# Performance work log

Hardware: AMD Instinct MI355X
Metric: run time of the kernel (lower is better)

The kernel has to match this reference:

```python
import jax, jax.numpy as jnp
import numpy as np

B, C, H, W = 4, 256, 48, 48
HEADS, DIM_HEAD, SCALE = 8, 64, 10.0
INNER = HEADS * DIM_HEAD
EPS = 1e-12


def setup_inputs() -> dict:
    key = jax.random.key(0)
    k1, k2, k3, k4 = jax.random.split(key, 4)
    x = jax.random.normal(k1, (B, C, H, W), dtype=jnp.float32)
    # 1x1 conv weights stored as [out_ch, in_ch]
    w_qkv = jax.random.normal(k2, (3 * INNER, C), dtype=jnp.float32) * (1.0 / np.sqrt(C))
    w_out = jax.random.normal(k3, (C, INNER), dtype=jnp.float32) * (1.0 / np.sqrt(INNER))
    b_out = jax.random.normal(k4, (C,), dtype=jnp.float32) * 0.01
    return {"x": x, "w_qkv": w_qkv, "w_out": w_out, "b_out": b_out}


def _l2norm(t):
    # normalize along last axis, clamping the norm at EPS (matches torch l2norm)
    denom = jnp.maximum(jnp.linalg.norm(t, axis=-1, keepdims=True), EPS)
    return t / denom


def reference(x, w_qkv, w_out, b_out):
    b, c, h, w = x.shape
    n = h * w
    # 1x1 conv QKV projection: [B, 3*INNER, H, W]
    qkv = jnp.einsum('oc,bchw->bohw', w_qkv, x)
    q, k, v = jnp.split(qkv, 3, axis=1)
    # [B, heads, dim_head, N] -> [B, heads, N, dim_head]
    def to_bhnd(t):
        return t.reshape(b, HEADS, DIM_HEAD, n).transpose(0, 1, 3, 2)
    q = _l2norm(to_bhnd(q))
    k = _l2norm(to_bhnd(k))
    v = to_bhnd(v)
    sim = jnp.einsum('bhid,bhjd->bhij', q, k) * SCALE  # [B,h,N,N]
    attn = jax.nn.softmax(sim, axis=-1)
    out = jnp.einsum('bhij,bhjd->bhid', attn, v)  # [B,h,N,d]
    # back to [B, INNER, H, W]
    out = out.transpose(0, 1, 3, 2).reshape(b, INNER, h, w)
    # 1x1 conv output projection with bias
    out = jnp.einsum('oc,bchw->bohw', w_out, out) + b_out[None, :, None, None]
    return out
```

## Files before the change

### kernel.cpp

```cpp
#include <hip/hip_runtime.h>

typedef unsigned short u16;
typedef __attribute__((ext_vector_type(8))) short bf16x8;
typedef __attribute__((ext_vector_type(4))) float f32x4;

#define MFMA16(A,B,C) __builtin_amdgcn_mfma_f32_16x16x32_bf16(A,B,C,0,0,0)

#define B_ 4
#define C_ 256
#define N_ 2304
#define HEADS_ 8
#define DH_ 64
#define INNER_ 512
#define SCALE_LOG2E 14.426950408889634f

__device__ __forceinline__ u16 f2bf(float f) {
    union { float f; unsigned int u; } v; v.f = f;
    unsigned int r = v.u + 0x7fffu + ((v.u >> 16) & 1u);
    return (u16)(r >> 16);
}
__device__ __forceinline__ unsigned int pk2(float a, float b) {
    union { float f; unsigned int u; } va, vb; va.f = a; vb.f = b;
    return __builtin_amdgcn_perm(vb.u + 0x8000u, va.u + 0x8000u, 0x07060302u);
}

__global__ __launch_bounds__(256) void k_prep(const float* __restrict__ x,
                                              u16* __restrict__ xT,
                                              const float* __restrict__ w_qkv,
                                              u16* __restrict__ wqb,
                                              const float* __restrict__ w_out,
                                              u16* __restrict__ wob) {
    __shared__ float tile[64][65];
    int idx = blockIdx.x;
    int t = threadIdx.x;
    if (idx < 576) {
        int b = idx / 144, rem = idx % 144;
        int n0 = (rem >> 2) * 64, c0 = (rem & 3) * 64;
        const float* xb = x + (size_t)b * C_ * N_;
        u16* xTb = xT + (size_t)b * N_ * C_;
        int r = t >> 4;
        int q4 = (t & 15) * 4;
#pragma unroll
        for (int pass = 0; pass < 4; ++pass) {
            int c = r + pass * 16;
            float4 v = *(const float4*)(xb + (size_t)(c0 + c) * N_ + n0 + q4);
            tile[c][q4+0] = v.x; tile[c][q4+1] = v.y; tile[c][q4+2] = v.z; tile[c][q4+3] = v.w;
        }
        __syncthreads();
#pragma unroll
        for (int pass = 0; pass < 4; ++pass) {
            int n = r + pass * 16;
            ushort4 o;
            o.x = f2bf(tile[q4+0][n]); o.y = f2bf(tile[q4+1][n]);
            o.z = f2bf(tile[q4+2][n]); o.w = f2bf(tile[q4+3][n]);
            *(ushort4*)(xTb + (size_t)(n0 + n) * C_ + c0 + q4) = o;
        }
    } else if (idx < 960) {
        int i = (idx - 576) * 256 + t;
        float4 v = ((const float4*)w_qkv)[i];
        ushort4 o;
        o.x = f2bf(v.x); o.y = f2bf(v.y); o.z = f2bf(v.z); o.w = f2bf(v.w);
        ((ushort4*)wqb)[i] = o;
    } else {
        int i = (idx - 960) * 256 + t;
        float4 v = ((const float4*)w_out)[i];
        ushort4 o;
        o.x = f2bf(v.x); o.y = f2bf(v.y); o.z = f2bf(v.z); o.w = f2bf(v.w);
        ((ushort4*)wob)[i] = o;
    }
}

__global__ __launch_bounds__(256) void k_qkv(const u16* __restrict__ w_qkv,
                                             const u16* __restrict__ xT,
                                             u16* __restrict__ Qn,
                                             u16* __restrict__ Kn,
                                             u16* __restrict__ Vt) {
    __shared__ __align__(16) u16 Wt[64][264];
    __shared__ __align__(16) u16 Xt[64][264];
    int mt = blockIdx.x, nt = blockIdx.y, b = blockIdx.z;
    int tid = threadIdx.x;
    int wv = tid >> 6, lane = tid & 63;
    int col = lane & 15, quad = lane >> 4;
    int o0 = mt * 64;
    const u16* wtile = w_qkv + (size_t)o0 * C_;
    const u16* xtile = xT + ((size_t)b * N_ + nt*64) * C_;
#pragma unroll
    for (int p = 0; p < 8; ++p) {
        int c = p * 256 + tid;
        int row = c >> 5, seg = c & 31;
        *(uint4*)(&Wt[row][seg*8]) = *(const uint4*)(wtile + (size_t)row * C_ + seg*8);
        *(uint4*)(&Xt[row][seg*8]) = *(const uint4*)(xtile + (size_t)row * C_ + seg*8);
    }
    __syncthreads();
    f32x4 z = {0.f, 0.f, 0.f, 0.f};
    f32x4 acc[4]; acc[0]=z; acc[1]=z; acc[2]=z; acc[3]=z;
#pragma unroll
    for (int ks = 0; ks < 8; ++ks) {
        bf16x8 bfrag = *(const bf16x8*)(&Xt[wv*16 + col][ks*32 + quad*8]);
#pragma unroll
        for (int mb = 0; mb < 4; ++mb) {
            bf16x8 afrag = *(const bf16x8*)(&Wt[mb*16 + col][ks*32 + quad*8]);
            acc[mb] = MFMA16(afrag, bfrag, acc[mb]);
        }
    }
    int n = nt * 64 + wv * 16 + col;
    int which = mt >> 3, h = mt & 7;
    if (which < 2) {
        float s = 0.f;
#pragma unroll
        for (int mb = 0; mb < 4; ++mb)
#pragma unroll
            for (int r = 0; r < 4; ++r) s += acc[mb][r] * acc[mb][r];
        s += __shfl_xor(s, 16);
        s += __shfl_xor(s, 32);
        float inv = 1.f / fmaxf(sqrtf(s), 1e-12f);
        u16* dst = (which == 0 ? Qn : Kn) + (((size_t)b * HEADS_ + h) * N_ + n) * DH_;
#pragma unroll
        for (int mb = 0; mb < 4; ++mb) {
            ushort4 o;
            o.x = f2bf(acc[mb][0] * inv); o.y = f2bf(acc[mb][1] * inv);
            o.z = f2bf(acc[mb][2] * inv); o.w = f2bf(acc[mb][3] * inv);
            *(ushort4*)(dst + mb*16 + quad*4) = o;
        }
    } else {
        u16* dst = Vt + ((size_t)b * HEADS_ + h) * (size_t)DH_ * N_;
#pragma unroll
        for (int mb = 0; mb < 4; ++mb)
#pragma unroll
            for (int r = 0; r < 4; ++r)
                dst[(size_t)(mb*16 + quad*4 + r) * N_ + n] = f2bf(acc[mb][r]);
    }
}

__global__ __launch_bounds__(256) void k_attn_split(const u16* __restrict__ Qn,
                                                    const u16* __restrict__ Kn,
                                                    const u16* __restrict__ Vt,
                                                    float* __restrict__ Op,
                                                    float* __restrict__ lp) {
    __shared__ __align__(16) u16 Kt[64][72];
    __shared__ __align__(16) u16 Vtl[64][72];
    __shared__ __align__(16) u16 plds[4][32][72];
    int head_lin = blockIdx.x & 31;
    int rest = blockIdx.x >> 5;
    int qt = rest % 18;
    int khalf = rest / 18;
    int b = head_lin >> 3, h = head_lin & 7;
    int tid = threadIdx.x;
    int wv = tid >> 6, lane = tid & 63;
    int col = lane & 15, quad = lane >> 4;
    size_t head = (size_t)b * HEADS_ + h;
    const u16* Qh = Qn + head * (size_t)N_ * DH_;
    const u16* Kh = Kn + head * (size_t)N_ * DH_ + (size_t)khalf * 1152 * DH_;
    const u16* Vh = Vt + head * (size_t)DH_ * N_;
    int q0 = qt * 128 + wv * 32;
    bf16x8 qfA0 = *(const bf16x8*)(Qh + (size_t)(q0 + col) * DH_ + quad*8);
    bf16x8 qfA1 = *(const bf16x8*)(Qh + (size_t)(q0 + col) * DH_ + 32 + quad*8);
    bf16x8 qfB0 = *(const bf16x8*)(Qh + (size_t)(q0 + 16 + col) * DH_ + quad*8);
    bf16x8 qfB1 = *(const bf16x8*)(Qh + (size_t)(q0 + 16 + col) * DH_ + 32 + quad*8);
    f32x4 z = {0.f, 0.f, 0.f, 0.f};
    f32x4 OA[4], OB[4];
#pragma unroll
    for (int i = 0; i < 4; ++i) { OA[i] = z; OB[i] = z; }
    float lA = 0.f, lB = 0.f;
    int srow = tid >> 3, sseg = tid & 7;
    const u16* ksrc0 = Kh + (size_t)tid * 8;
    const u16* vsrc0 = Vh + (size_t)srow * N_ + khalf * 1152 + sseg * 8;

    uint4 k0 = *(const uint4*)(ksrc0);
    uint4 k1 = *(const uint4*)(ksrc0 + 2048);
    uint4 v0 = *(const uint4*)(vsrc0);
    uint4 v1 = *(const uint4*)(vsrc0 + (size_t)32 * N_);

    for (int kt = 0; kt < 18; ++kt) {
        *(uint4*)(&Kt[srow][sseg*8])      = k0;
        *(uint4*)(&Kt[32 + srow][sseg*8]) = k1;
        *(uint4*)(&Vtl[srow][sseg*8])      = v0;
        *(uint4*)(&Vtl[32 + srow][sseg*8]) = v1;
        __syncthreads();
        int ktn = kt + 1 < 18 ? kt + 1 : kt;
        k0 = *(const uint4*)(ksrc0 + (size_t)ktn * 4096);
        k1 = *(const uint4*)(ksrc0 + (size_t)ktn * 4096 + 2048);
        v0 = *(const uint4*)(vsrc0 + ktn * 64);
        v1 = *(const uint4*)(vsrc0 + (size_t)32 * N_ + ktn * 64);
        float rsA = 0.f, rsB = 0.f;
#pragma unroll
        for (int nb = 0; nb < 4; ++nb) {
            bf16x8 kf0 = *(const bf16x8*)(&Kt[nb*16 + col][quad*8]);
            bf16x8 kf1 = *(const bf16x8*)(&Kt[nb*16 + col][32 + quad*8]);
            f32x4 a = MFMA16(kf0, qfA0, z);
            a = MFMA16(kf1, qfA1, a);
            f32x4 c = MFMA16(kf0, qfB0, z);
            c = MFMA16(kf1, qfB1, c);
            float a0 = exp2f(fmaf(a[0], SCALE_LOG2E, -SCALE_LOG2E));
            float a1 = exp2f(fmaf(a[1], SCALE_LOG2E, -SCALE_LOG2E));
            float a2 = exp2f(fmaf(a[2], SCALE_LOG2E, -SCALE_LOG2E));
            float a3 = exp2f(fmaf(a[3], SCALE_LOG2E, -SCALE_LOG2E));
            float c0 = exp2f(fmaf(c[0], SCALE_LOG2E, -SCALE_LOG2E));
            float c1 = exp2f(fmaf(c[1], SCALE_LOG2E, -SCALE_LOG2E));
            float c2 = exp2f(fmaf(c[2], SCALE_LOG2E, -SCALE_LOG2E));
            float c3 = exp2f(fmaf(c[3], SCALE_LOG2E, -SCALE_LOG2E));
            rsA += (a0 + a1) + (a2 + a3);
            rsB += (c0 + c1) + (c2 + c3);
            uint2 wA, wB;
            wA.x = pk2(a0, a1); wA.y = pk2(a2, a3);
            wB.x = pk2(c0, c1); wB.y = pk2(c2, c3);
            *(uint2*)(&plds[wv][col][nb*16 + quad*4]) = wA;
            *(uint2*)(&plds[wv][16 + col][nb*16 + quad*4]) = wB;
        }
        lA += rsA; lB += rsB;
        __asm__ volatile("" ::: "memory");
#pragma unroll
        for (int ks = 0; ks < 2; ++ks) {
            bf16x8 pfA = *(const bf16x8*)(&plds[wv][col][ks*32 + quad*8]);
            bf16x8 pfB = *(const bf16x8*)(&plds[wv][16 + col][ks*32 + quad*8]);
#pragma unroll
            for (int nb = 0; nb < 4; ++nb) {
                bf16x8 vf = *(const bf16x8*)(&Vtl[nb*16 + col][ks*32 + quad*8]);
                OA[nb] = MFMA16(vf, pfA, OA[nb]);
                OB[nb] = MFMA16(vf, pfB, OB[nb]);
            }
        }
        __asm__ volatile("" ::: "memory");
        __syncthreads();
    }
    lA += __shfl_xor(lA, 16); lA += __shfl_xor(lA, 32);
    lB += __shfl_xor(lB, 16); lB += __shfl_xor(lB, 32);
    float* dstA = Op + (((size_t)khalf * B_ + b) * N_ + q0 + col) * INNER_ + h * DH_;
    float* dstB = dstA + (size_t)16 * INNER_;
#pragma unroll
    for (int nb = 0; nb < 4; ++nb) {
        *(f32x4*)(dstA + nb*16 + quad*4) = OA[nb];
        *(f32x4*)(dstB + nb*16 + quad*4) = OB[nb];
    }
    if (quad == 0) {
        size_t lbase = (((size_t)khalf * B_ + b) * HEADS_ + h) * N_;
        lp[lbase + q0 + col] = lA;
        lp[lbase + q0 + 16 + col] = lB;
    }
}

__global__ __launch_bounds__(256) void k_comb(const float* __restrict__ Op,
                                              const float* __restrict__ lp,
                                              u16* __restrict__ AO) {
    int g = blockIdx.x * 256 + threadIdx.x;
    int b = g / 294912;
    int rem = g % 294912;
    int n = rem >> 7;
    int i4 = rem & 127;
    int h = i4 >> 4;
    float4 a = ((const float4*)Op)[g];
    float4 c = ((const float4*)Op)[g + 1179648];
    float l = lp[((size_t)b * HEADS_ + h) * N_ + n] +
              lp[(((size_t)B_ + b) * HEADS_ + h) * N_ + n];
    float inv = 1.f / l;
    ushort4 o;
    o.x = f2bf((a.x + c.x) * inv);
    o.y = f2bf((a.y + c.y) * inv);
    o.z = f2bf((a.z + c.z) * inv);
    o.w = f2bf((a.w + c.w) * inv);
    ((ushort4*)AO)[g] = o;
}

__global__ __launch_bounds__(256) void k_attn(const u16* __restrict__ Qn,
                                              const u16* __restrict__ Kn,
                                              const u16* __restrict__ Vt,
                                              u16* __restrict__ AO) {
    __shared__ __align__(16) u16 Kt[64][72];
    __shared__ __align__(16) u16 Vtl[64][72];
    __shared__ __align__(16) u16 plds[4][32][72];
    int head_lin = blockIdx.x & 31;
    int qt = blockIdx.x >> 5;
    int b = head_lin >> 3, h = head_lin & 7;
    int tid = threadIdx.x;
    int wv = tid >> 6, lane = tid & 63;
    int col = lane & 15, quad = lane >> 4;
    size_t head = (size_t)b * HEADS_ + h;
    const u16* Qh = Qn + head * (size_t)N_ * DH_;
    const u16* Kh = Kn + head * (size_t)N_ * DH_;
    const u16* Vh = Vt + head * (size_t)DH_ * N_;
    int q0 = qt * 128 + wv * 32;
    bf16x8 qfA0 = *(const bf16x8*)(Qh + (size_t)(q0 + col) * DH_ + quad*8);
    bf16x8 qfA1 = *(const bf16x8*)(Qh + (size_t)(q0 + col) * DH_ + 32 + quad*8);
    bf16x8 qfB0 = *(const bf16x8*)(Qh + (size_t)(q0 + 16 + col) * DH_ + quad*8);
    bf16x8 qfB1 = *(const bf16x8*)(Qh + (size_t)(q0 + 16 + col) * DH_ + 32 + quad*8);
    f32x4 z = {0.f, 0.f, 0.f, 0.f};
    f32x4 OA[4], OB[4];
#pragma unroll
    for (int i = 0; i < 4; ++i) { OA[i] = z; OB[i] = z; }
    float lA = 0.f, lB = 0.f;
    int srow = tid >> 3, sseg = tid & 7;
    const u16* ksrc0 = Kh + (size_t)tid * 8;
    const u16* vsrc0 = Vh + (size_t)srow * N_ + sseg * 8;

    uint4 k0 = *(const uint4*)(ksrc0);
    uint4 k1 = *(const uint4*)(ksrc0 + 2048);
    uint4 v0 = *(const uint4*)(vsrc0);
    uint4 v1 = *(const uint4*)(vsrc0 + (size_t)32 * N_);

    for (int kt = 0; kt < N_/64; ++kt) {
        *(uint4*)(&Kt[srow][sseg*8])      = k0;
        *(uint4*)(&Kt[32 + srow][sseg*8]) = k1;
        *(uint4*)(&Vtl[srow][sseg*8])      = v0;
        *(uint4*)(&Vtl[32 + srow][sseg*8]) = v1;
        __syncthreads();
        int ktn = kt + 1 < N_/64 ? kt + 1 : kt;
        k0 = *(const uint4*)(ksrc0 + (size_t)ktn * 4096);
        k1 = *(const uint4*)(ksrc0 + (size_t)ktn * 4096 + 2048);
        v0 = *(const uint4*)(vsrc0 + ktn * 64);
        v1 = *(const uint4*)(vsrc0 + (size_t)32 * N_ + ktn * 64);
        float rsA = 0.f, rsB = 0.f;
#pragma unroll
        for (int nb = 0; nb < 4; ++nb) {
            bf16x8 kf0 = *(const bf16x8*)(&Kt[nb*16 + col][quad*8]);
            bf16x8 kf1 = *(const bf16x8*)(&Kt[nb*16 + col][32 + quad*8]);
            f32x4 a = MFMA16(kf0, qfA0, z);
            a = MFMA16(kf1, qfA1, a);
            f32x4 c = MFMA16(kf0, qfB0, z);
            c = MFMA16(kf1, qfB1, c);
            float a0 = exp2f(fmaf(a[0], SCALE_LOG2E, -SCALE_LOG2E));
            float a1 = exp2f(fmaf(a[1], SCALE_LOG2E, -SCALE_LOG2E));
            float a2 = exp2f(fmaf(a[2], SCALE_LOG2E, -SCALE_LOG2E));
            float a3 = exp2f(fmaf(a[3], SCALE_LOG2E, -SCALE_LOG2E));
            float c0 = exp2f(fmaf(c[0], SCALE_LOG2E, -SCALE_LOG2E));
            float c1 = exp2f(fmaf(c[1], SCALE_LOG2E, -SCALE_LOG2E));
            float c2 = exp2f(fmaf(c[2], SCALE_LOG2E, -SCALE_LOG2E));
            float c3 = exp2f(fmaf(c[3], SCALE_LOG2E, -SCALE_LOG2E));
            rsA += (a0 + a1) + (a2 + a3);
            rsB += (c0 + c1) + (c2 + c3);
            uint2 wA, wB;
            wA.x = pk2(a0, a1); wA.y = pk2(a2, a3);
            wB.x = pk2(c0, c1); wB.y = pk2(c2, c3);
            *(uint2*)(&plds[wv][col][nb*16 + quad*4]) = wA;
            *(uint2*)(&plds[wv][16 + col][nb*16 + quad*4]) = wB;
        }
        lA += rsA; lB += rsB;
        __asm__ volatile("" ::: "memory");
#pragma unroll
        for (int ks = 0; ks < 2; ++ks) {
            bf16x8 pfA = *(const bf16x8*)(&plds[wv][col][ks*32 + quad*8]);
            bf16x8 pfB = *(const bf16x8*)(&plds[wv][16 + col][ks*32 + quad*8]);
#pragma unroll
            for (int nb = 0; nb < 4; ++nb) {
                bf16x8 vf = *(const bf16x8*)(&Vtl[nb*16 + col][ks*32 + quad*8]);
                OA[nb] = MFMA16(vf, pfA, OA[nb]);
                OB[nb] = MFMA16(vf, pfB, OB[nb]);
            }
        }
        __asm__ volatile("" ::: "memory");
        __syncthreads();
    }
    lA += __shfl_xor(lA, 16); lA += __shfl_xor(lA, 32);
    lB += __shfl_xor(lB, 16); lB += __shfl_xor(lB, 32);
    float linvA = 1.f / lA, linvB = 1.f / lB;
    u16* dstA = AO + ((size_t)b * N_ + q0 + col) * INNER_ + h * DH_;
    u16* dstB = AO + ((size_t)b * N_ + q0 + 16 + col) * INNER_ + h * DH_;
#pragma unroll
    for (int nb = 0; nb < 4; ++nb) {
        uint2 wA, wB;
        wA.x = pk2(OA[nb][0] * linvA, OA[nb][1] * linvA);
        wA.y = pk2(OA[nb][2] * linvA, OA[nb][3] * linvA);
        wB.x = pk2(OB[nb][0] * linvB, OB[nb][1] * linvB);
        wB.y = pk2(OB[nb][2] * linvB, OB[nb][3] * linvB);
        *(uint2*)(dstA + nb*16 + quad*4) = wA;
        *(uint2*)(dstB + nb*16 + quad*4) = wB;
    }
}

__global__ __launch_bounds__(256) void k_proj(const u16* __restrict__ w_out,
                                              const float* __restrict__ b_out,
                                              const u16* __restrict__ AO,
                                              float* __restrict__ out) {
    __shared__ __align__(16) u16 Wt[64][264];
    __shared__ __align__(16) u16 At[64][264];
    int mt = blockIdx.x, nt = blockIdx.y, b = blockIdx.z;
    int tid = threadIdx.x;
    int wv = tid >> 6, lane = tid & 63;
    int col = lane & 15, quad = lane >> 4;
    int o0b = mt * 64;
    const u16* wtile = w_out + (size_t)o0b * INNER_;
    const u16* atile = AO + ((size_t)b * N_ + nt*64) * INNER_;
    f32x4 z = {0.f, 0.f, 0.f, 0.f};
    f32x4 acc[4]; acc[0]=z; acc[1]=z; acc[2]=z; acc[3]=z;
#pragma unroll
    for (int half = 0; half < 2; ++half) {
        if (half) __syncthreads();
#pragma unroll
        for (int p = 0; p < 8; ++p) {
            int c = p * 256 + tid;
            int row = c >> 5, seg = c & 31;
            *(uint4*)(&Wt[row][seg*8]) =
                *(const uint4*)(wtile + (size_t)row * INNER_ + half*256 + seg*8);
            *(uint4*)(&At[row][seg*8]) =
                *(const uint4*)(atile + (size_t)row * INNER_ + half*256 + seg*8);
        }
        __syncthreads();
#pragma unroll
        for (int ks = 0; ks < 8; ++ks) {
            bf16x8 af = *(const bf16x8*)(&Wt[wv*16 + col][ks*32 + quad*8]);
#pragma unroll
            for (int nb = 0; nb < 4; ++nb) {
                bf16x8 bfv = *(const bf16x8*)(&At[nb*16 + col][ks*32 + quad*8]);
                acc[nb] = MFMA16(af, bfv, acc[nb]);
            }
        }
    }
    int o0 = o0b + wv * 16;
    float bias[4];
#pragma unroll
    for (int r = 0; r < 4; ++r) bias[r] = b_out[o0 + quad*4 + r];
    float* dst = out + ((size_t)b * C_ + o0) * N_ + nt*64;
#pragma unroll
    for (int nb = 0; nb < 4; ++nb)
#pragma unroll
        for (int r = 0; r < 4; ++r)
            dst[(size_t)(quad*4 + r) * N_ + nb*16 + col] = acc[nb][r] + bias[r];
}

extern "C" void kernel_launch(void* const* d_in, const int* in_sizes, int n_in,
                              void* d_out, int out_size, void* d_ws, size_t ws_size,
                              hipStream_t stream) {
    const float* x     = (const float*)d_in[0];
    const float* w_qkv = (const float*)d_in[1];
    const float* w_out = (const float*)d_in[2];
    const float* b_out = (const float*)d_in[3];
    float* out = (float*)d_out;

    char* ws = (char*)d_ws;
    u16* xT  = (u16*)(ws);
    u16* Qn  = (u16*)(ws + 4718592);
    u16* Kn  = (u16*)(ws + 14155776);
    u16* Vt  = (u16*)(ws + 23592960);
    u16* AO  = (u16*)(ws + 33030144);
    u16* wqb = (u16*)(ws + 42467328);
    u16* wob = (u16*)(ws + 43253760);
    float* Op = (float*)(ws + 43515904);
    float* lp = (float*)(ws + 81264640);
    const size_t need = 81854464;

    hipLaunchKernelGGL(k_prep, dim3(1088), dim3(256), 0, stream, x, xT, w_qkv, wqb, w_out, wob);
    hipLaunchKernelGGL(k_qkv,  dim3(24, N_/64, B_), dim3(256), 0, stream, wqb, xT, Qn, Kn, Vt);
    if (ws_size >= need) {
        hipLaunchKernelGGL(k_attn_split, dim3(1152), dim3(256), 0, stream, Qn, Kn, Vt, Op, lp);
        hipLaunchKernelGGL(k_comb, dim3(4608), dim3(256), 0, stream, Op, lp, AO);
    } else {
        hipLaunchKernelGGL(k_attn, dim3((N_/128) * 32), dim3(256), 0, stream, Qn, Kn, Vt, AO);
    }
    hipLaunchKernelGGL(k_proj, dim3(C_/64, N_/64, B_), dim3(256), 0, stream, wob, b_out, AO, out);
}
```

Baseline: 196.3 us.

## Split attention keys four ways and store bf16 partial outputs

The split-key attention kernel now divides the 2304 keys into four chunks of 576 instead of two halves, doubling the grid to 2304 blocks. Partial outputs are packed to bf16 instead of fp32, and the combine kernel sums four bf16 partials and four row-sum terms before normalising. The aim is better load balance and occupancy across CUs without raising partial-buffer traffic. In exchange, each Q tile is loaded twice as often, the combine reads more streams, and rounding unnormalised partials to bf16 loses accuracy. The row-sum buffer is moved into the xT workspace region, which is no longer needed once the QKV projection has run.

```diff
diff --git a/kernel.cpp b/kernel.cpp
--- a/kernel.cpp
+++ b/kernel.cpp
@@ -18,6 +18,10 @@
     union { float f; unsigned int u; } v; v.f = f;
     unsigned int r = v.u + 0x7fffu + ((v.u >> 16) & 1u);
     return (u16)(r >> 16);
+}
+__device__ __forceinline__ float bf2f(u16 h) {
+    union { unsigned int u; float f; } v; v.u = ((unsigned int)h) << 16;
+    return v.f;
 }
 __device__ __forceinline__ unsigned int pk2(float a, float b) {
     union { float f; unsigned int u; } va, vb; va.f = a; vb.f = b;
@@ -135,7 +139,7 @@
 __global__ __launch_bounds__(256) void k_attn_split(const u16* __restrict__ Qn,
                                                     const u16* __restrict__ Kn,
                                                     const u16* __restrict__ Vt,
-                                                    float* __restrict__ Op,
+                                                    u16* __restrict__ Opb,
                                                     float* __restrict__ lp) {
     __shared__ __align__(16) u16 Kt[64][72];
     __shared__ __align__(16) u16 Vtl[64][72];
@@ -143,14 +147,14 @@
     int head_lin = blockIdx.x & 31;
     int rest = blockIdx.x >> 5;
     int qt = rest % 18;
-    int khalf = rest / 18;
+    int ksplit = rest / 18;
     int b = head_lin >> 3, h = head_lin & 7;
     int tid = threadIdx.x;
     int wv = tid >> 6, lane = tid & 63;
     int col = lane & 15, quad = lane >> 4;
     size_t head = (size_t)b * HEADS_ + h;
     const u16* Qh = Qn + head * (size_t)N_ * DH_;
-    const u16* Kh = Kn + head * (size_t)N_ * DH_ + (size_t)khalf * 1152 * DH_;
+    const u16* Kh = Kn + head * (size_t)N_ * DH_ + (size_t)ksplit * 576 * DH_;
     const u16* Vh = Vt + head * (size_t)DH_ * N_;
     int q0 = qt * 128 + wv * 32;
     bf16x8 qfA0 = *(const bf16x8*)(Qh + (size_t)(q0 + col) * DH_ + quad*8);
@@ -164,20 +168,20 @@
     float lA = 0.f, lB = 0.f;
     int srow = tid >> 3, sseg = tid & 7;
     const u16* ksrc0 = Kh + (size_t)tid * 8;
-    const u16* vsrc0 = Vh + (size_t)srow * N_ + khalf * 1152 + sseg * 8;
+    const u16* vsrc0 = Vh + (size_t)srow * N_ + ksplit * 576 + sseg * 8;
 
     uint4 k0 = *(const uint4*)(ksrc0);
     uint4 k1 = *(const uint4*)(ksrc0 + 2048);
     uint4 v0 = *(const uint4*)(vsrc0);
     uint4 v1 = *(const uint4*)(vsrc0 + (size_t)32 * N_);
 
-    for (int kt = 0; kt < 18; ++kt) {
+    for (int kt = 0; kt < 9; ++kt) {
         *(uint4*)(&Kt[srow][sseg*8])      = k0;
         *(uint4*)(&Kt[32 + srow][sseg*8]) = k1;
         *(uint4*)(&Vtl[srow][sseg*8])      = v0;
         *(uint4*)(&Vtl[32 + srow][sseg*8]) = v1;
         __syncthreads();
-        int ktn = kt + 1 < 18 ? kt + 1 : kt;
+        int ktn = kt + 1 < 9 ? kt + 1 : kt;
         k0 = *(const uint4*)(ksrc0 + (size_t)ktn * 4096);
         k1 = *(const uint4*)(ksrc0 + (size_t)ktn * 4096 + 2048);
         v0 = *(const uint4*)(vsrc0 + ktn * 64);
@@ -225,21 +229,24 @@
     }
     lA += __shfl_xor(lA, 16); lA += __shfl_xor(lA, 32);
     lB += __shfl_xor(lB, 16); lB += __shfl_xor(lB, 32);
-    float* dstA = Op + (((size_t)khalf * B_ + b) * N_ + q0 + col) * INNER_ + h * DH_;
-    float* dstB = dstA + (size_t)16 * INNER_;
+    u16* dstA = Opb + (((size_t)ksplit * B_ + b) * N_ + q0 + col) * INNER_ + h * DH_;
+    u16* dstB = dstA + (size_t)16 * INNER_;
 #pragma unroll
     for (int nb = 0; nb < 4; ++nb) {
-        *(f32x4*)(dstA + nb*16 + quad*4) = OA[nb];
-        *(f32x4*)(dstB + nb*16 + quad*4) = OB[nb];
+        uint2 wA, wB;
+        wA.x = pk2(OA[nb][0], OA[nb][1]); wA.y = pk2(OA[nb][2], OA[nb][3]);
+        wB.x = pk2(OB[nb][0], OB[nb][1]); wB.y = pk2(OB[nb][2], OB[nb][3]);
+        *(uint2*)(dstA + nb*16 + quad*4) = wA;
+        *(uint2*)(dstB + nb*16 + quad*4) = wB;
     }
     if (quad == 0) {
-        size_t lbase = (((size_t)khalf * B_ + b) * HEADS_ + h) * N_;
+        size_t lbase = (((size_t)ksplit * B_ + b) * HEADS_ + h) * N_;
         lp[lbase + q0 + col] = lA;
         lp[lbase + q0 + 16 + col] = lB;
     }
 }
 
-__global__ __launch_bounds__(256) void k_comb(const float* __restrict__ Op,
+__global__ __launch_bounds__(256) void k_comb(const u16* __restrict__ Opb,
                                               const float* __restrict__ lp,
                                               u16* __restrict__ AO) {
     int g = blockIdx.x * 256 + threadIdx.x;
@@ -248,16 +255,17 @@
     int n = rem >> 7;
     int i4 = rem & 127;
     int h = i4 >> 4;
-    float4 a = ((const float4*)Op)[g];
-    float4 c = ((const float4*)Op)[g + 1179648];
-    float l = lp[((size_t)b * HEADS_ + h) * N_ + n] +
-              lp[(((size_t)B_ + b) * HEADS_ + h) * N_ + n];
+    float s0 = 0.f, s1 = 0.f, s2 = 0.f, s3 = 0.f, l = 0.f;
+#pragma unroll
+    for (int s = 0; s < 4; ++s) {
+        ushort4 p = ((const ushort4*)Opb)[g + (size_t)s * 1179648];
+        s0 += bf2f(p.x); s1 += bf2f(p.y); s2 += bf2f(p.z); s3 += bf2f(p.w);
+        l += lp[(((size_t)s * B_ + b) * HEADS_ + h) * N_ + n];
+    }
     float inv = 1.f / l;
     ushort4 o;
-    o.x = f2bf((a.x + c.x) * inv);
-    o.y = f2bf((a.y + c.y) * inv);
-    o.z = f2bf((a.z + c.z) * inv);
-    o.w = f2bf((a.w + c.w) * inv);
+    o.x = f2bf(s0 * inv); o.y = f2bf(s1 * inv);
+    o.z = f2bf(s2 * inv); o.w = f2bf(s3 * inv);
     ((ushort4*)AO)[g] = o;
 }
 
@@ -291,12 +299,10 @@
     int srow = tid >> 3, sseg = tid & 7;
     const u16* ksrc0 = Kh + (size_t)tid * 8;
     const u16* vsrc0 = Vh + (size_t)srow * N_ + sseg * 8;
-
     uint4 k0 = *(const uint4*)(ksrc0);
     uint4 k1 = *(const uint4*)(ksrc0 + 2048);
     uint4 v0 = *(const uint4*)(vsrc0);
     uint4 v1 = *(const uint4*)(vsrc0 + (size_t)32 * N_);
-
     for (int kt = 0; kt < N_/64; ++kt) {
         *(uint4*)(&Kt[srow][sseg*8])      = k0;
         *(uint4*)(&Kt[32 + srow][sseg*8]) = k1;
@@ -433,15 +439,15 @@
     u16* AO  = (u16*)(ws + 33030144);
     u16* wqb = (u16*)(ws + 42467328);
     u16* wob = (u16*)(ws + 43253760);
-    float* Op = (float*)(ws + 43515904);
-    float* lp = (float*)(ws + 81264640);
+    u16* Opb = (u16*)(ws + 43515904);
+    float* lp = (float*)(ws + 1179648);
     const size_t need = 81854464;
 
     hipLaunchKernelGGL(k_prep, dim3(1088), dim3(256), 0, stream, x, xT, w_qkv, wqb, w_out, wob);
     hipLaunchKernelGGL(k_qkv,  dim3(24, N_/64, B_), dim3(256), 0, stream, wqb, xT, Qn, Kn, Vt);
     if (ws_size >= need) {
-        hipLaunchKernelGGL(k_attn_split, dim3(1152), dim3(256), 0, stream, Qn, Kn, Vt, Op, lp);
-        hipLaunchKernelGGL(k_comb, dim3(4608), dim3(256), 0, stream, Op, lp, AO);
+        hipLaunchKernelGGL(k_attn_split, dim3(2304), dim3(256), 0, stream, Qn, Kn, Vt, Opb, lp);
+        hipLaunchKernelGGL(k_comb, dim3(4608), dim3(256), 0, stream, Opb, lp, AO);
     } else {
         hipLaunchKernelGGL(k_attn, dim3((N_/128) * 32), dim3(256), 0, stream, Qn, Kn, Vt, AO);
     }
```

Result: faster. 190.7 us (-2.8%).
